# Kernel tuning notes

Measured on AMD Instinct MI355X. Metric: run time of the kernel, lower is better.

Reference implementation:

```python
import jax, jax.numpy as jnp
import numpy as np

B, C, H, W = 16, 256, 32, 32
N_EMBED = 8192
BETA = 0.25


def setup_inputs() -> dict:
    key = jax.random.key(0)
    k1, k2 = jax.random.split(key)
    x = jax.random.normal(k1, (B, C, H, W), dtype=jnp.float32)
    # nn.Embedding(n_embed + 1, dim); last row is the padding row (unused by argmin path)
    weight = jax.random.normal(k2, (N_EMBED + 1, C), dtype=jnp.float32) * 0.01
    return {"x": x, "weight": weight}


def reference(x, weight):
    b, c, h, w = x.shape
    codebook = weight[:-1, :]                      # [n_embed, d]
    xt = jnp.transpose(x, (0, 2, 3, 1)).reshape(b, h * w, c)   # b (h w) c
    flat = xt.reshape(-1, c)                       # [N, d]

    x_sq = jnp.sum(flat * flat, axis=1, keepdims=True)          # [N, 1]
    c_sq = jnp.sum(codebook * codebook, axis=1)[None, :]        # [1, n_embed]
    dists = x_sq + c_sq - 2.0 * (flat @ codebook.T)             # [N, n_embed]
    code = jnp.argmin(dists, axis=-1)                           # [N]

    x_q = codebook[code]                                        # gather [N, d]
    x_q = x_q.reshape(b, h * w, c)
    code = code.reshape(b, h * w)

    # commitment losses (eval mode: no EMA buffer update)
    sg = jax.lax.stop_gradient
    loss = BETA * jnp.mean((sg(x_q) - xt) ** 2) + jnp.mean((x_q - sg(xt)) ** 2)

    # straight-through estimator
    x_q = xt + sg(x_q - xt)

    x_q = jnp.transpose(x_q.reshape(b, h, w, c), (0, 3, 1, 2))  # b c h w
    code = code.reshape(b, h, w)
    return x_q, loss, code
```

## Files before the change

### kernel.cpp

```cpp
#include <hip/hip_runtime.h>
#include <float.h>
#include <limits.h>
#include <math.h>

#define B_      16
#define C_      256
#define HW      1024
#define ROWS    (B_*HW)
#define NCODE   8192
#define KDIM    256

#define SXQ 28.0f
#define SWQ 2400.0f
#define SPROD_HALF 33600.0

typedef __attribute__((ext_vector_type(4)))  int i32x4;
typedef __attribute__((ext_vector_type(16))) int i32x16;

__device__ __forceinline__ unsigned umn(unsigned a, unsigned b){ return a < b ? a : b; }
__device__ __forceinline__ unsigned umx(unsigned a, unsigned b){ return a > b ? a : b; }

__device__ __forceinline__ void gload_lds16(const void* g, void* l) {
    __builtin_amdgcn_global_load_lds(
        (const __attribute__((address_space(1))) unsigned int*)g,
        (__attribute__((address_space(3))) unsigned int*)l, 16, 0, 0);
}

__device__ __forceinline__ uint4 merge44(uint4 a, uint4 b) {
    unsigned w0 = umn(a.x, b.w), w1 = umn(a.y, b.z);
    unsigned w2 = umn(a.z, b.y), w3 = umn(a.w, b.x);
    unsigned s0 = umn(w0, w2), s2 = umx(w0, w2);
    unsigned s1 = umn(w1, w3), s3 = umx(w1, w3);
    uint4 o;
    o.x = umn(s0, s1); o.y = umx(s0, s1);
    o.z = umn(s2, s3); o.w = umx(s2, s3);
    return o;
}

__device__ __forceinline__ int q8(float v, float s) {
    return __float2int_rn(fminf(fmaxf(v * s, -127.f), 127.f));
}

__global__ __launch_bounds__(256)
void prep_kernel(const float* __restrict__ x, const float* __restrict__ w,
                 float* __restrict__ csq, unsigned char* __restrict__ wq8,
                 unsigned char* __restrict__ xq8)
{
    __shared__ float Lt[64][65];

    if (blockIdx.x < 2048) {
        int j = blockIdx.x * 4 + (threadIdx.x >> 6);
        int l = threadIdx.x & 63;
        float4 v = *(const float4*)(w + (size_t)j * KDIM + l * 4);
        double s = (double)v.x*v.x + (double)v.y*v.y + (double)v.z*v.z + (double)v.w*v.w;
        #pragma unroll
        for (int off = 1; off < 64; off <<= 1) s += __shfl_xor(s, off, 64);
        if (l == 0) csq[j] = (float)s;

        int q0 = q8(v.x, SWQ), q1 = q8(v.y, SWQ), q2 = q8(v.z, SWQ), q3 = q8(v.w, SWQ);
        unsigned pk = (unsigned)(q0 & 0xFF) | ((unsigned)(q1 & 0xFF) << 8)
                    | ((unsigned)(q2 & 0xFF) << 16) | ((unsigned)(q3 & 0xFF) << 24);
        int k32 = l >> 3, hi = (l >> 2) & 1, idx = (l & 3) * 4;
        int cb = j >> 5;
        *(unsigned*)(wq8 + ((size_t)(k32 * 256 + cb) * 64 + (j & 31) + 32 * hi) * 16 + idx) = pk;

        if (l < 2) {
            double T = -s * SPROD_HALF;
            int wA = (int)rint(T / 127.0);
            int wB = (int)rint(T - 127.0 * (double)wA);
            wA = wA < -127 ? -127 : (wA > 127 ? 127 : wA);
            wB = wB < -127 ? -127 : (wB > 127 ? 127 : wB);
            uint4 f; f.x = 0; f.y = 0; f.z = 0; f.w = 0;
            if (l == 0) f.x = (unsigned)(wA & 0xFF) | ((unsigned)(wB & 0xFF) << 8);
            *(uint4*)(wq8 + ((size_t)(8 * 256 + cb) * 64 + (j & 31) + 32 * l) * 16) = f;
        }
        return;
    }

    int bx = blockIdx.x - 2048;
    int t  = threadIdx.x;
    int b  = bx >> 6;
    int kt = (bx >> 4) & 3;
    int pt = bx & 15;

    #pragma unroll
    for (int rnd = 0; rnd < 16; ++rnd) {
        int kk = rnd * 4 + (t >> 6);
        int pp = t & 63;
        Lt[kk][pp] = x[((size_t)(b * 256 + kt * 64 + kk)) * 1024 + pt * 64 + pp];
    }
    __syncthreads();

    int p = t >> 2, q = t & 3;
    int row = b * 1024 + pt * 64 + p;
    int xb  = row >> 5;
    int k32 = kt * 2 + (q >> 1), hi = q & 1;

    unsigned wds[4];
    #pragma unroll
    for (int wi = 0; wi < 4; ++wi) {
        unsigned pk = 0;
        #pragma unroll
        for (int i2 = 0; i2 < 4; ++i2) {
            int qi = q8(Lt[q*16 + wi*4 + i2][p], SXQ);
            pk |= ((unsigned)(qi & 0xFF)) << (8 * i2);
        }
        wds[wi] = pk;
    }
    uint4 pkv; pkv.x = wds[0]; pkv.y = wds[1]; pkv.z = wds[2]; pkv.w = wds[3];
    *(uint4*)(xq8 + ((size_t)(k32 * 512 + xb) * 64 + (p & 31) + 32 * hi) * 16) = pkv;

    if (kt == 0 && q < 2) {
        uint4 f; f.x = 0; f.y = 0; f.z = 0; f.w = 0;
        if (q == 0) f.x = 127u | (1u << 8);
        *(uint4*)(xq8 + ((size_t)(8 * 512 + xb) * 64 + (p & 31) + 32 * q) * 16) = f;
    }
}

__global__ __launch_bounds__(256, 2)
void stage1_kernel(const unsigned char* __restrict__ wq8,
                   const unsigned char* __restrict__ xq8,
                   uint4* __restrict__ part)
{
    extern __shared__ unsigned char smem[];
    unsigned char* slot = smem;

    const int tid = threadIdx.x;
    const int wid = tid >> 6;
    const int l   = tid & 63;
    const int bid = blockIdx.x;
    const int chunk = (bid & 7) >> 1;
    const int rb    = (bid >> 3) | ((bid & 1) << 6);
    const int row0  = rb * 128;
    const int cbase = chunk * 2048;
    const int wr = wid >> 1, wc = wid & 1;

    i32x4 xf[9][2];
    #pragma unroll
    for (int k9 = 0; k9 < 9; ++k9)
        #pragma unroll
        for (int nf = 0; nf < 2; ++nf)
            xf[k9][nf] = *(const i32x4*)(xq8 +
                ((size_t)(k9 * 512 + rb * 4 + wc * 2 + nf) * 64 + l) * 16);

    auto stage3 = [&](int tt, int qq, int bb) {
        #pragma unroll
        for (int j = 0; j < 3; ++j) {
            int kk = 3 * qq + j;
            #pragma unroll
            for (int c = 0; c < 2; ++c) {
                int cbrel = wid * 2 + c;
                size_t src = (((size_t)(kk * 256 + chunk * 64 + tt * 8 + cbrel)) * 64 + l) * 16;
                gload_lds16(wq8 + src, slot + bb * 24576 + j * 8192 + cbrel * 1024);
            }
        }
    };

    stage3(0, 0, 0);
    stage3(0, 1, 1);
    asm volatile("s_waitcnt vmcnt(6)" ::: "memory");
    __builtin_amdgcn_s_barrier();
    __builtin_amdgcn_sched_barrier(0);

    unsigned key1[2], key2[2], key3[2];
    key1[0]=0xFFFFFFFFu; key1[1]=0xFFFFFFFFu;
    key2[0]=0xFFFFFFFFu; key2[1]=0xFFFFFFFFu;
    key3[0]=0xFFFFFFFFu; key3[1]=0xFFFFFFFFu;
    const int hi4 = (l >> 5) * 4;

    #pragma unroll 1
    for (int t = 0; t < 8; ++t) {
        i32x16 acc[4][2];
        #pragma unroll
        for (int mf = 0; mf < 4; ++mf)
            #pragma unroll
            for (int nf = 0; nf < 2; ++nf)
                acc[mf][nf] = (i32x16)(0);

        #pragma unroll
        for (int q = 0; q < 3; ++q) {
            if (q == 0)               stage3(t,     2, 2);
            else if (q == 1) { if (t < 7) stage3(t + 1, 0, 0); }
            else             { if (t < 7) stage3(t + 1, 1, 1); }

            #pragma unroll
            for (int j = 0; j < 3; ++j) {
                const int k9 = 3 * q + j;
                const unsigned char* Ac = slot + q * 24576 + j * 8192;
                i32x4 af[4];
                #pragma unroll
                for (int mf = 0; mf < 4; ++mf)
                    af[mf] = *(const i32x4*)(Ac + (wr * 4 + mf) * 1024 + l * 16);
                __builtin_amdgcn_s_setprio(1);
                #pragma unroll
                for (int mf = 0; mf < 4; ++mf)
                    #pragma unroll
                    for (int nf = 0; nf < 2; ++nf)
                        acc[mf][nf] = __builtin_amdgcn_mfma_i32_32x32x32_i8(
                            af[mf], xf[k9][nf], acc[mf][nf], 0, 0, 0);
                __builtin_amdgcn_s_setprio(0);
            }

            if (q == 2) {
                #pragma unroll
                for (int mf = 0; mf < 4; ++mf) {
                    unsigned base_mf = (unsigned)(t * 256 + (wr * 4 + mf) * 32 + hi4);
                    #pragma unroll
                    for (int nf = 0; nf < 2; ++nf) {
                        #pragma unroll
                        for (int j2 = 0; j2 < 4; ++j2) {
                            unsigned k0 = ((unsigned)(0x100000 - acc[mf][nf][4*j2+0]) << 11) | (base_mf + 8*j2 + 0);
                            unsigned k1 = ((unsigned)(0x100000 - acc[mf][nf][4*j2+1]) << 11) | (base_mf + 8*j2 + 1);
                            unsigned k2 = ((unsigned)(0x100000 - acc[mf][nf][4*j2+2]) << 11) | (base_mf + 8*j2 + 2);
                            unsigned k3 = ((unsigned)(0x100000 - acc[mf][nf][4*j2+3]) << 11) | (base_mf + 8*j2 + 3);
                            unsigned qm = umn(umn(k0, k1), umn(k2, k3));
                            unsigned t1 = umn(key1[nf], qm), t2 = umx(key1[nf], qm);
                            key1[nf] = t1;
                            unsigned u1 = umn(key2[nf], t2), u2 = umx(key2[nf], t2);
                            key2[nf] = u1;
                            key3[nf] = umn(key3[nf], u2);
                        }
                    }
                }
            }

            if (!(t == 7 && q == 2)) {
                if (t < 7 || q == 0) asm volatile("s_waitcnt vmcnt(6)" ::: "memory");
                else                 asm volatile("s_waitcnt vmcnt(0)" ::: "memory");
                __builtin_amdgcn_s_barrier();
                __builtin_amdgcn_sched_barrier(0);
            }
        }
    }

    __syncthreads();

    uint4* red = (uint4*)slot;
    #pragma unroll
    for (int nf = 0; nf < 2; ++nf) {
        unsigned a1 = key1[nf], a2 = key2[nf], a3 = key3[nf];
        unsigned b1 = __shfl_xor(a1, 32, 64);
        unsigned b2 = __shfl_xor(a2, 32, 64);
        unsigned b3 = __shfl_xor(a3, 32, 64);
        uint4 av; av.x = a1; av.y = a2; av.z = a3; av.w = 0xFFFFFFFFu;
        uint4 bv; bv.x = b1; bv.y = b2; bv.z = b3; bv.w = 0xFFFFFFFFu;
        uint4 m = merge44(av, bv);
        if (l < 32) {
            int xrl = (wc * 2 + nf) * 32 + (l & 31);
            red[xrl * 2 + wr] = m;
        }
    }
    __syncthreads();

    if (tid < 128) {
        uint4 m = merge44(red[tid * 2 + 0], red[tid * 2 + 1]);
        uint4 o;
        o.x = (unsigned)cbase + (m.x & 0x7FFu);
        o.y = (unsigned)cbase + (m.y & 0x7FFu);
        o.z = (unsigned)cbase + (m.z & 0x7FFu);
        o.w = (unsigned)cbase + (m.w & 0x7FFu);
        part[(size_t)(row0 + tid) * 4 + chunk] = o;
    }
}

__global__ __launch_bounds__(256)
void tail_kernel(const float* __restrict__ x, const float* __restrict__ w,
                 const float* __restrict__ csq, const unsigned* __restrict__ part,
                 float* __restrict__ xq, float* __restrict__ code_f,
                 double* __restrict__ partials)
{
    extern __shared__ unsigned char sm2[];
    float*    Lt    = (float*)sm2;
    float*    Wt    = (float*)(sm2 + 33792);
    unsigned* PcL   = (unsigned*)(sm2 + 33792 + 33280);
    int*      codeL = (int*)(sm2 + 33792 + 33280 + 2048);

    const int tid = threadIdx.x;
    const int b   = blockIdx.x >> 5;
    const int p0  = (blockIdx.x & 31) * 32;

    #pragma unroll 4
    for (int it = 0; it < 32; ++it) {
        int c  = it * 8 + (tid >> 5);
        int pp = tid & 31;
        Lt[c * 33 + pp] = x[((size_t)(b * 256 + c)) * 1024 + p0 + pp];
    }
    {
        const unsigned* ps = part + (size_t)(b * 1024 + p0) * 16;
        *(uint2*)&PcL[tid * 2] = *(const uint2*)&ps[tid * 2];
    }
    __syncthreads();

    const int w4   = tid >> 6;
    const int lane = tid & 63;
    const int pr   = lane >> 3, s = lane & 7;
    const int rl   = w4 * 8 + pr;

    float xs[32];
    #pragma unroll
    for (int k = 0; k < 32; ++k) xs[k] = Lt[(s * 32 + k) * 33 + rl];

    double ss = 0.0;
    #pragma unroll
    for (int k = 0; k < 32; ++k) ss += (double)xs[k] * (double)xs[k];
    ss += __shfl_xor(ss, 1, 64);
    ss += __shfl_xor(ss, 2, 64);
    ss += __shfl_xor(ss, 4, 64);
    float S32 = (float)ss;

    float bd = FLT_MAX; int bi = INT_MAX;
    #pragma unroll 1
    for (int ct = 0; ct < 16; ++ct) {
        int ci = (int)PcL[rl * 16 + ct];
        const float4* wr4 = (const float4*)(w + (size_t)ci * 256 + s * 32);
        float csv = csq[ci];
        double acc = 0.0;
        #pragma unroll
        for (int q4 = 0; q4 < 8; ++q4) {
            float4 wv = wr4[q4];
            acc += (double)wv.x * (double)xs[q4*4 + 0];
            acc += (double)wv.y * (double)xs[q4*4 + 1];
            acc += (double)wv.z * (double)xs[q4*4 + 2];
            acc += (double)wv.w * (double)xs[q4*4 + 3];
        }
        acc += __shfl_xor(acc, 1, 64);
        acc += __shfl_xor(acc, 2, 64);
        acc += __shfl_xor(acc, 4, 64);
        float tt = (float)(2.0 * acc);
        float sc = S32 + csv;
        float d  = sc - tt;
        if (d < bd || (d == bd && ci < bi)) { bd = d; bi = ci; }
    }
    if (s == 0) {
        codeL[rl] = bi;
        code_f[b * 1024 + p0 + rl] = (float)bi;
    }
    __syncthreads();

    #pragma unroll
    for (int it = 0; it < 8; ++it) {
        int r2 = it * 4 + w4;
        int code = codeL[r2];
        float4 wv = *(const float4*)(w + (size_t)code * 256 + lane * 4);
        *(float4*)&Wt[r2 * 260 + lane * 4] = wv;
    }
    __syncthreads();

    double ls = 0.0;
    #pragma unroll 4
    for (int it = 0; it < 32; ++it) {
        int c  = it * 8 + (tid >> 5);
        int pp = tid & 31;
        float val = Wt[pp * 260 + c];
        float xv  = Lt[c * 33 + pp];
        xq[((size_t)(b * 256 + c)) * 1024 + p0 + pp] = val;
        float diff = val - xv;
        ls += (double)diff * (double)diff;
    }
    #pragma unroll
    for (int off = 1; off < 64; off <<= 1) ls += __shfl_xor(ls, off, 64);
    if (lane == 0) partials[blockIdx.x * 4 + w4] = ls;
}

__global__ __launch_bounds__(256)
void loss_kernel(const double* __restrict__ partials, float* __restrict__ loss_out)
{
    __shared__ double sred[256];
    double s = 0.0;
    for (int i = threadIdx.x; i < 2048; i += 256) s += partials[i];
    sred[threadIdx.x] = s;
    __syncthreads();
    for (int k = 128; k > 0; k >>= 1) {
        if (threadIdx.x < k) sred[threadIdx.x] += sred[threadIdx.x + k];
        __syncthreads();
    }
    if (threadIdx.x == 0)
        loss_out[0] = (float)(sred[0] * (1.25 / (double)(B_ * 256 * HW)));
}

extern "C" void kernel_launch(void* const* d_in, const int* in_sizes, int n_in,
                              void* d_out, int out_size, void* d_ws, size_t ws_size,
                              hipStream_t stream)
{
    const float* x = (const float*)d_in[0];
    const float* w = (const float*)d_in[1];
    float* out    = (float*)d_out;
    float* xq     = out;
    float* loss   = out + 4194304;
    float* code_f = out + 4194305;

    char* ws = (char*)d_ws;
    float*         csq      = (float*)(ws);
    double*        partials = (double*)(ws + 256*1024);
    uint4*         part     = (uint4*)(ws + 512*1024);
    unsigned char* wq8      = (unsigned char*)(ws + (size_t)2*1024*1024);
    unsigned char* xq8      = (unsigned char*)(ws + (size_t)5*1024*1024);

    (void)hipFuncSetAttribute((const void*)stage1_kernel,
                              hipFuncAttributeMaxDynamicSharedMemorySize, 73728);
    (void)hipFuncSetAttribute((const void*)tail_kernel,
                              hipFuncAttributeMaxDynamicSharedMemorySize, 69248);

    prep_kernel   <<<3072,  256, 0, stream>>>(x, w, csq, wq8, xq8);
    stage1_kernel <<<512,   256, 73728, stream>>>(wq8, xq8, part);
    tail_kernel   <<<512,   256, 69248, stream>>>(x, w, csq, (const unsigned*)part,
                                                  xq, code_f, partials);
    loss_kernel   <<<1,     256, 0, stream>>>(partials, loss);
}
```

Before: 102.0 us.

## Give each wave a private LDS ring to remove block-wide barriers in stage1

In stage1, the shared LDS staging buffer that all four waves filled cooperatively and synchronized with block barriers is replaced by a 4-slot ring private to each wave. Each wave now loads only the codebook fragments it consumes, one k-slice at a time, prefetching three slices ahead and using only vmcnt waits instead of s_barrier. This removes cross-wave synchronization stalls and trims LDS from 72KB to 64KB. The cost is that rows shared between the two waves with the same wr are now loaded twice, and the s_setprio hints around the MFMA blocks are dropped.

```diff
diff --git a/kernel.cpp b/kernel.cpp
--- a/kernel.cpp
+++ b/kernel.cpp
@@ -123,8 +123,6 @@
                    uint4* __restrict__ part)
 {
     extern __shared__ unsigned char smem[];
-    unsigned char* slot = smem;
-
     const int tid = threadIdx.x;
     const int wid = tid >> 6;
     const int l   = tid & 63;
@@ -134,6 +132,7 @@
     const int row0  = rb * 128;
     const int cbase = chunk * 2048;
     const int wr = wid >> 1, wc = wid & 1;
+    unsigned char* priv = smem + wid * 16384;
 
     i32x4 xf[9][2];
     #pragma unroll
@@ -142,25 +141,19 @@
         for (int nf = 0; nf < 2; ++nf)
             xf[k9][nf] = *(const i32x4*)(xq8 +
                 ((size_t)(k9 * 512 + rb * 4 + wc * 2 + nf) * 64 + l) * 16);
-
-    auto stage3 = [&](int tt, int qq, int bb) {
-        #pragma unroll
-        for (int j = 0; j < 3; ++j) {
-            int kk = 3 * qq + j;
-            #pragma unroll
-            for (int c = 0; c < 2; ++c) {
-                int cbrel = wid * 2 + c;
-                size_t src = (((size_t)(kk * 256 + chunk * 64 + tt * 8 + cbrel)) * 64 + l) * 16;
-                gload_lds16(wq8 + src, slot + bb * 24576 + j * 8192 + cbrel * 1024);
-            }
+    asm volatile("s_waitcnt vmcnt(0)" ::: "memory");
+
+    auto stage1p = [&](int tt, int kk, int sl) {
+        #pragma unroll
+        for (int mf = 0; mf < 4; ++mf) {
+            size_t src = (((size_t)(kk * 256 + chunk * 64 + tt * 8 + wr * 4 + mf)) * 64 + l) * 16;
+            gload_lds16(wq8 + src, priv + sl * 4096 + mf * 1024);
         }
     };
 
-    stage3(0, 0, 0);
-    stage3(0, 1, 1);
-    asm volatile("s_waitcnt vmcnt(6)" ::: "memory");
-    __builtin_amdgcn_s_barrier();
-    __builtin_amdgcn_sched_barrier(0);
+    stage1p(0, 0, 0);
+    stage1p(0, 1, 1);
+    stage1p(0, 2, 2);
 
     unsigned key1[2], key2[2], key3[2];
     key1[0]=0xFFFFFFFFu; key1[1]=0xFFFFFFFFu;
@@ -178,64 +171,63 @@
                 acc[mf][nf] = (i32x16)(0);
 
         #pragma unroll
-        for (int q = 0; q < 3; ++q) {
-            if (q == 0)               stage3(t,     2, 2);
-            else if (q == 1) { if (t < 7) stage3(t + 1, 0, 0); }
-            else             { if (t < 7) stage3(t + 1, 1, 1); }
-
+        for (int k9 = 0; k9 < 9; ++k9) {
+            {
+                int k2 = k9 + 3, t2 = t;
+                if (k2 >= 9) { k2 -= 9; t2 = t + 1; }
+                if (k9 < 6 || t < 7) stage1p(t2, k2, (t + k9 + 3) & 3);
+            }
+            if (k9 < 6) {
+                asm volatile("s_waitcnt vmcnt(12)" ::: "memory");
+            } else if (t < 7) {
+                asm volatile("s_waitcnt vmcnt(12)" ::: "memory");
+            } else if (k9 == 6) {
+                asm volatile("s_waitcnt vmcnt(8)" ::: "memory");
+            } else if (k9 == 7) {
+                asm volatile("s_waitcnt vmcnt(4)" ::: "memory");
+            } else {
+                asm volatile("s_waitcnt vmcnt(0)" ::: "memory");
+            }
+            __builtin_amdgcn_sched_barrier(0);
+
+            const unsigned char* Ac = priv + ((t + k9) & 3) * 4096;
+            i32x4 af[4];
             #pragma unroll
-            for (int j = 0; j < 3; ++j) {
-                const int k9 = 3 * q + j;
-                const unsigned char* Ac = slot + q * 24576 + j * 8192;
-                i32x4 af[4];
+            for (int mf = 0; mf < 4; ++mf)
+                af[mf] = *(const i32x4*)(Ac + mf * 1024 + l * 16);
+            #pragma unroll
+            for (int mf = 0; mf < 4; ++mf)
                 #pragma unroll
-                for (int mf = 0; mf < 4; ++mf)
-                    af[mf] = *(const i32x4*)(Ac + (wr * 4 + mf) * 1024 + l * 16);
-                __builtin_amdgcn_s_setprio(1);
+                for (int nf = 0; nf < 2; ++nf)
+                    acc[mf][nf] = __builtin_amdgcn_mfma_i32_32x32x32_i8(
+                        af[mf], xf[k9][nf], acc[mf][nf], 0, 0, 0);
+        }
+
+        #pragma unroll
+        for (int mf = 0; mf < 4; ++mf) {
+            unsigned base_mf = (unsigned)(t * 256 + (wr * 4 + mf) * 32 + hi4);
+            #pragma unroll
+            for (int nf = 0; nf < 2; ++nf) {
                 #pragma unroll
-                for (int mf = 0; mf < 4; ++mf)
-                    #pragma unroll
-                    for (int nf = 0; nf < 2; ++nf)
-                        acc[mf][nf] = __builtin_amdgcn_mfma_i32_32x32x32_i8(
-                            af[mf], xf[k9][nf], acc[mf][nf], 0, 0, 0);
-                __builtin_amdgcn_s_setprio(0);
-            }
-
-            if (q == 2) {
-                #pragma unroll
-                for (int mf = 0; mf < 4; ++mf) {
-                    unsigned base_mf = (unsigned)(t * 256 + (wr * 4 + mf) * 32 + hi4);
-                    #pragma unroll
-                    for (int nf = 0; nf < 2; ++nf) {
-                        #pragma unroll
-                        for (int j2 = 0; j2 < 4; ++j2) {
-                            unsigned k0 = ((unsigned)(0x100000 - acc[mf][nf][4*j2+0]) << 11) | (base_mf + 8*j2 + 0);
-                            unsigned k1 = ((unsigned)(0x100000 - acc[mf][nf][4*j2+1]) << 11) | (base_mf + 8*j2 + 1);
-                            unsigned k2 = ((unsigned)(0x100000 - acc[mf][nf][4*j2+2]) << 11) | (base_mf + 8*j2 + 2);
-                            unsigned k3 = ((unsigned)(0x100000 - acc[mf][nf][4*j2+3]) << 11) | (base_mf + 8*j2 + 3);
-                            unsigned qm = umn(umn(k0, k1), umn(k2, k3));
-                            unsigned t1 = umn(key1[nf], qm), t2 = umx(key1[nf], qm);
-                            key1[nf] = t1;
-                            unsigned u1 = umn(key2[nf], t2), u2 = umx(key2[nf], t2);
-                            key2[nf] = u1;
-                            key3[nf] = umn(key3[nf], u2);
-                        }
-                    }
+                for (int j2 = 0; j2 < 4; ++j2) {
+                    unsigned k0 = ((unsigned)(0x100000 - acc[mf][nf][4*j2+0]) << 11) | (base_mf + 8*j2 + 0);
+                    unsigned k1 = ((unsigned)(0x100000 - acc[mf][nf][4*j2+1]) << 11) | (base_mf + 8*j2 + 1);
+                    unsigned k2 = ((unsigned)(0x100000 - acc[mf][nf][4*j2+2]) << 11) | (base_mf + 8*j2 + 2);
+                    unsigned k3 = ((unsigned)(0x100000 - acc[mf][nf][4*j2+3]) << 11) | (base_mf + 8*j2 + 3);
+                    unsigned qm = umn(umn(k0, k1), umn(k2, k3));
+                    unsigned t1 = umn(key1[nf], qm), t2 = umx(key1[nf], qm);
+                    key1[nf] = t1;
+                    unsigned u1 = umn(key2[nf], t2), u2 = umx(key2[nf], t2);
+                    key2[nf] = u1;
+                    key3[nf] = umn(key3[nf], u2);
                 }
             }
-
-            if (!(t == 7 && q == 2)) {
-                if (t < 7 || q == 0) asm volatile("s_waitcnt vmcnt(6)" ::: "memory");
-                else                 asm volatile("s_waitcnt vmcnt(0)" ::: "memory");
-                __builtin_amdgcn_s_barrier();
-                __builtin_amdgcn_sched_barrier(0);
-            }
-        }
-    }
-
-    __syncthreads();
-
-    uint4* red = (uint4*)slot;
+        }
+    }
+
+    __syncthreads();
+
+    uint4* red = (uint4*)smem;
     #pragma unroll
     for (int nf = 0; nf < 2; ++nf) {
         unsigned a1 = key1[nf], a2 = key2[nf], a3 = key3[nf];
@@ -397,12 +389,12 @@
     unsigned char* xq8      = (unsigned char*)(ws + (size_t)5*1024*1024);
 
     (void)hipFuncSetAttribute((const void*)stage1_kernel,
-                              hipFuncAttributeMaxDynamicSharedMemorySize, 73728);
+                              hipFuncAttributeMaxDynamicSharedMemorySize, 65536);
     (void)hipFuncSetAttribute((const void*)tail_kernel,
                               hipFuncAttributeMaxDynamicSharedMemorySize, 69248);
 
     prep_kernel   <<<3072,  256, 0, stream>>>(x, w, csq, wq8, xq8);
-    stage1_kernel <<<512,   256, 73728, stream>>>(wq8, xq8, part);
+    stage1_kernel <<<512,   256, 65536, stream>>>(wq8, xq8, part);
     tail_kernel   <<<512,   256, 69248, stream>>>(x, w, csq, (const unsigned*)part,
                                                   xq, code_f, partials);
     loss_kernel   <<<1,     256, 0, stream>>>(partials, loss);
```

Measured after the change: 103.5 us. About the same (+1.5%).
